# Optimization experiments

Measured on AMD Instinct MI355X. Metric: run time of the kernel, lower is better.

Reference implementation:

```python
import jax, jax.numpy as jnp
import numpy as np

D_MODEL = 768
N_HEADS = 12
D_HEAD = D_MODEL // N_HEADS


def setup_inputs() -> dict:
    key = jax.random.key(0)
    k_x, k_qw, k_qb, k_ow, k_ob = jax.random.split(key, 5)
    B, N = 2, 4096
    scale = 1.0 / np.sqrt(D_MODEL)
    return {
        "x": jax.random.normal(k_x, (B, N, D_MODEL), dtype=jnp.float32),
        # torch nn.Linear stores weight as [out_features, in_features]
        "qkv_w": jax.random.uniform(k_qw, (3 * D_MODEL, D_MODEL), jnp.float32, -scale, scale),
        "qkv_b": jax.random.uniform(k_qb, (3 * D_MODEL,), jnp.float32, -scale, scale),
        "out_w": jax.random.uniform(k_ow, (D_MODEL, D_MODEL), jnp.float32, -scale, scale),
        "out_b": jax.random.uniform(k_ob, (D_MODEL,), jnp.float32, -scale, scale),
    }


def reference(x, qkv_w, qkv_b, out_w, out_b):
    B, N, D = x.shape
    qkv = x @ qkv_w.T + qkv_b                                   # [B, N, 3D]
    qkv = qkv.reshape(B, N, 3, N_HEADS, D_HEAD)
    qkv = jnp.transpose(qkv, (2, 0, 3, 1, 4))                    # [3, B, H, N, d]
    q, k, v = qkv[0], qkv[1], qkv[2]
    scores = jnp.einsum("bhqd,bhkd->bhqk", q, k) / np.sqrt(D_HEAD)
    attn = jax.nn.softmax(scores, axis=-1)
    out = jnp.einsum("bhqk,bhkd->bhqd", attn, v)                 # [B, H, N, d]
    out = jnp.transpose(out, (0, 2, 1, 3)).reshape(B, N, D)
    return out @ out_w.T + out_b
```

## Files before the change

### kernel.cpp

```cpp
#include <hip/hip_runtime.h>
#include <cstdint>

#define SEQ 4096
#define NH 12
#define DH 64
#define DM 768
#define MT 8192
#define QKVN 2304

typedef __bf16 bf16;
typedef __attribute__((ext_vector_type(8))) __bf16 bf16x8;
typedef __attribute__((ext_vector_type(4))) __bf16 bf16x4;
typedef __attribute__((ext_vector_type(2))) __bf16 bf16x2;
typedef __attribute__((ext_vector_type(4))) float f32x4;
typedef __attribute__((ext_vector_type(16))) float f32x16;
typedef __attribute__((ext_vector_type(2))) int int2v;

__device__ __forceinline__ void async_ld16(const void* g, void* lds) {
  __builtin_amdgcn_global_load_lds(
      (__attribute__((address_space(1))) void*)(void*)g,
      (__attribute__((address_space(3))) void*)lds, 16, 0, 0);
}

__device__ __forceinline__ int pexp2_pair(float s0, float s1) {
  int j0 = (int)__builtin_fmaf(s0, 128.0f, 16251.5f);
  int j1 = (int)__builtin_fmaf(s1, 128.0f, 16251.5f);
  return j0 | (j1 << 16);
}

__device__ __forceinline__ void lane32_swap(int& a, int& b) {
#if __has_builtin(__builtin_amdgcn_permlane32_swap)
  int2v r = __builtin_amdgcn_permlane32_swap(a, b, false, false);
  a = r.x; b = r.y;
#else
  int hi = (threadIdx.x & 63) >> 5;
  int ra = __shfl_xor(a, 32, 64), rb = __shfl_xor(b, 32, 64);
  int na = hi ? rb : a;
  int nb = hi ? b : ra;
  a = na; b = nb;
#endif
}

#define NX4  (MT * DM / 4)
#define NW14 (QKVN * DM / 4)
#define NW24 (DM * DM / 4)
__global__ void cvt_all(const float* __restrict__ x, const float* __restrict__ w1,
                        const float* __restrict__ w2, bf16* __restrict__ xb,
                        bf16* __restrict__ wb1, bf16* __restrict__ wb2) {
  int i = blockIdx.x * blockDim.x + threadIdx.x;
  const float* src; bf16* dst; int j;
  if (i < NX4) { src = x; dst = xb; j = i; }
  else if (i < NX4 + NW14) { src = w1; dst = wb1; j = i - NX4; }
  else if (i < NX4 + NW14 + NW24) { src = w2; dst = wb2; j = i - NX4 - NW14; }
  else return;
  f32x4 v = ((const f32x4*)src)[j];
  bf16x4 o;
  o.x = (bf16)v.x; o.y = (bf16)v.y; o.z = (bf16)v.z; o.w = (bf16)v.w;
  ((bf16x4*)dst)[j] = o;
}

template<int MODE>
__global__ __launch_bounds__(256) void gemm_bt(
    const bf16* __restrict__ A, const bf16* __restrict__ Bw,
    const float* __restrict__ bias,
    bf16* __restrict__ outQ, bf16* __restrict__ outK, bf16* __restrict__ outVt,
    float* __restrict__ outF,
    int M, int N, int K)
{
  __shared__ bf16 smem[2 * 128 * 64];
  bf16* sA = smem;
  bf16* sB = smem + 128 * 64;
  bf16* sT = smem;

  const int tid  = threadIdx.x;
  const int wave = tid >> 6;
  const int lane = tid & 63;
  const int l15  = lane & 15;
  const int quad = lane >> 4;

  constexpr int NT = (MODE == 0) ? (QKVN / 128) : (DM / 128);
  const int lin = blockIdx.x;
  const int rem = lin % (NT * 8);
  const int m0 = ((lin / (NT * 8)) * 8 + (rem % 8)) * 128;
  const int n0 = (rem / 8) * 128;

  const int rowbase = (wave >> 1) * 64;
  const int colbase = (wave & 1) * 64;

  f32x4 acc[4][4] = {};

  const int srow = lane >> 3;
  const int spg  = (lane & 7) ^ srow;
  const int xk   = l15 & 7;

  for (int kt = 0; kt < K; kt += 64) {
#pragma unroll
    for (int p = 0; p < 8; ++p) {
      int chunk = p * 4 + wave;
      if (chunk < 16) {
        int row = chunk * 8 + srow;
        async_ld16(A + (size_t)(m0 + row) * K + kt + spg * 8, &sA[chunk * 512]);
      } else {
        int row = (chunk - 16) * 8 + srow;
        async_ld16(Bw + (size_t)(n0 + row) * K + kt + spg * 8, &sB[(chunk - 16) * 512]);
      }
    }
    __syncthreads();

#pragma unroll
    for (int ks = 0; ks < 2; ++ks) {
      bf16x8 af[4], bfr[4];
#pragma unroll
      for (int rt = 0; rt < 4; ++rt)
        af[rt] = *(const bf16x8*)&sA[(rowbase + rt * 16 + l15) * 64 +
                                     (((ks * 4 + quad) ^ xk) * 8)];
#pragma unroll
      for (int ct = 0; ct < 4; ++ct)
        bfr[ct] = *(const bf16x8*)&sB[(colbase + ct * 16 + l15) * 64 +
                                      (((ks * 4 + quad) ^ xk) * 8)];
#pragma unroll
      for (int rt = 0; rt < 4; ++rt)
#pragma unroll
        for (int ct = 0; ct < 4; ++ct)
          acc[rt][ct] = __builtin_amdgcn_mfma_f32_16x16x32_bf16(af[rt], bfr[ct], acc[rt][ct], 0, 0, 0);
    }
    __syncthreads();
  }

  if (MODE == 0) {
    const int g = n0 / DM;
    if (g < 2) {
      const float qscale = 0.125f * 1.4426950408889634f;
#pragma unroll
      for (int ct = 0; ct < 4; ++ct) {
        int j = n0 + colbase + ct * 16 + l15;
        float bj = bias[j];
        int f = j % DM;
        int h = f >> 6, d = f & 63;
#pragma unroll
        for (int rt = 0; rt < 4; ++rt) {
          int mrow = m0 + rowbase + rt * 16 + quad * 4;
#pragma unroll
          for (int r = 0; r < 4; ++r) {
            float v = acc[rt][ct][r] + bj;
            int m = mrow + r;
            int b = m >> 12, n = m & 4095;
            int bh = b * NH + h;
            if (g == 0) outQ[((size_t)bh * SEQ + n) * DH + d] = (bf16)(v * qscale);
            else        outK[((size_t)bh * SEQ + n) * DH + d] = (bf16)v;
          }
        }
      }
    } else {
      const int f0 = n0 - 2 * DM;
      const int b = m0 >> 12, n0m = m0 & 4095;
#pragma unroll
      for (int p = 0; p < 2; ++p) {
        __syncthreads();
        if (colbase == p * 64) {
#pragma unroll
          for (int ct = 0; ct < 4; ++ct) {
            int jl = ct * 16 + l15;
            float bj = bias[n0 + p * 64 + jl];
#pragma unroll
            for (int rt = 0; rt < 4; ++rt) {
              int ml = rowbase + rt * 16 + quad * 4;
#pragma unroll
              for (int r = 0; r < 4; ++r)
                sT[jl * 136 + ml + r] = (bf16)(acc[rt][ct][r] + bj);
            }
          }
        }
        __syncthreads();
#pragma unroll
        for (int p2 = 0; p2 < 4; ++p2) {
          int slot = p2 * 256 + tid;
          int jr = slot >> 4, mc = (slot & 15) * 8;
          int fj = f0 + p * 64 + jr;
          int h = fj >> 6, d = fj & 63;
          *(bf16x8*)&outVt[((size_t)(b * NH + h) * DH + d) * SEQ + n0m + mc] =
              *(const bf16x8*)&sT[jr * 136 + mc];
        }
      }
    }
  } else {
#pragma unroll
    for (int ct = 0; ct < 4; ++ct) {
      int j = n0 + colbase + ct * 16 + l15;
      float bj = bias[j];
#pragma unroll
      for (int rt = 0; rt < 4; ++rt) {
        int mrow = m0 + rowbase + rt * 16 + quad * 4;
#pragma unroll
        for (int r = 0; r < 4; ++r)
          outF[(size_t)(mrow + r) * N + j] = acc[rt][ct][r] + bj;
      }
    }
  }
}

__global__ __launch_bounds__(256) void flash_attn(
    const bf16* __restrict__ Q, const bf16* __restrict__ Kg,
    const bf16* __restrict__ Vt, bf16* __restrict__ Oout)
{
  __shared__ bf16 sK[2][64 * 64];
  __shared__ bf16 sV[2][64 * 64];

  {
    int ph = (blockIdx.x + blockIdx.y) & 3;
    if (ph == 1) __builtin_amdgcn_s_sleep(2);
    else if (ph == 2) __builtin_amdgcn_s_sleep(4);
    else if (ph == 3) __builtin_amdgcn_s_sleep(6);
  }

  const int tid  = threadIdx.x;
  const int wave = tid >> 6;
  const int lane = tid & 63;
  const int l31  = lane & 31;
  const int hi   = lane >> 5;
  const int bh = blockIdx.y;
  const int q0w = blockIdx.x * 128 + wave * 32;

  const bf16* Qb = Q  + (size_t)bh * SEQ * DH;
  const bf16* Kb = Kg + (size_t)bh * SEQ * DH;
  const bf16* Vb = Vt + (size_t)bh * DH * SEQ;

  const int srow = lane >> 3;
  const int spg  = lane & 7;

  bf16x8 qf[4];
#pragma unroll
  for (int dc = 0; dc < 4; ++dc)
    qf[dc] = *(const bf16x8*)&Qb[(size_t)(q0w + l31) * DH + dc * 16 + hi * 8];

  bf16x8 ones1;
#pragma unroll
  for (int j = 0; j < 8; ++j) ones1[j] = (bf16)1.0f;

  f32x16 o0 = {}, o1 = {}, o2 = {};
  f32x16 zc = {};

  const int keyk = (l31 & 7) ^ (((l31 >> 3) & 3) << 1);
  int kOff[4], vOff[4];
#pragma unroll
  for (int dc = 0; dc < 4; ++dc)
    kOff[dc] = l31 * 64 + (((dc * 2 + hi) ^ keyk) * 8);
#pragma unroll
  for (int k4 = 0; k4 < 4; ++k4)
    vOff[k4] = l31 * 64 + (((k4 * 2 + hi) ^ keyk) * 8);

  auto stage = [&](int kt, int buf) {
#pragma unroll
    for (int j = 0; j < 2; ++j) {
      int r0 = wave * 16 + j * 8;
      int row = r0 + srow;
      int lg = spg ^ (row & 7) ^ (((row >> 3) & 3) << 1);
      async_ld16(Kb + (size_t)(kt + row) * DH + lg * 8, &sK[buf][r0 * 64]);
      async_ld16(Vb + (size_t)row * SEQ + kt + lg * 8, &sV[buf][r0 * 64]);
    }
  };

  auto compute = [&](const bf16* sKp, const bf16* sVp) {
#pragma unroll
    for (int kb = 0; kb < 2; ++kb) {
      f32x16 s;
      {
        bf16x8 kf = *(const bf16x8*)&sKp[kOff[0] + kb * 2048];
        s = __builtin_amdgcn_mfma_f32_32x32x16_bf16(kf, qf[0], zc, 0, 0, 0);
      }
#pragma unroll
      for (int dc = 1; dc < 4; ++dc) {
        bf16x8 kf = *(const bf16x8*)&sKp[kOff[dc] + kb * 2048];
        s = __builtin_amdgcn_mfma_f32_32x32x16_bf16(kf, qf[dc], s, 0, 0, 0);
      }
#pragma unroll
      for (int kc = 0; kc < 2; ++kc) {
        int g0a = pexp2_pair(s[8 * kc + 0], s[8 * kc + 1]);
        int g0b = pexp2_pair(s[8 * kc + 2], s[8 * kc + 3]);
        int g1a = pexp2_pair(s[8 * kc + 4], s[8 * kc + 5]);
        int g1b = pexp2_pair(s[8 * kc + 6], s[8 * kc + 7]);
        lane32_swap(g0a, g1a);
        lane32_swap(g0b, g1b);
        union { int i[4]; bf16x8 v; } Af;
        Af.i[0] = g0a; Af.i[1] = g0b; Af.i[2] = g1a; Af.i[3] = g1b;
        bf16x8 vf0 = *(const bf16x8*)&sVp[vOff[kb * 2 + kc]];
        bf16x8 vf1 = *(const bf16x8*)&sVp[vOff[kb * 2 + kc] + 2048];
        o0 = __builtin_amdgcn_mfma_f32_32x32x16_bf16(Af.v, vf0, o0, 0, 0, 0);
        o1 = __builtin_amdgcn_mfma_f32_32x32x16_bf16(Af.v, vf1, o1, 0, 0, 0);
        o2 = __builtin_amdgcn_mfma_f32_32x32x16_bf16(Af.v, ones1, o2, 0, 0, 0);
      }
    }
  };

  stage(0, 0);
  __syncthreads();

  for (int kt = 0; kt < SEQ; kt += 128) {
    if (kt + 64 < SEQ) stage(kt + 64, 1);
    compute(sK[0], sV[0]);
    __syncthreads();
    if (kt + 128 < SEQ) stage(kt + 128, 0);
    compute(sK[1], sV[1]);
    __syncthreads();
  }

  const int bg = bh / NH, h = bh % NH;
#pragma unroll
  for (int i = 0; i < 16; ++i) {
    int ql = 8 * (i >> 2) + (i & 3) + 4 * hi;
    float inv = 1.0f / o2[i];
    size_t base = (size_t)(bg * SEQ + q0w + ql) * DM + h * DH;
    Oout[base + l31]      = (bf16)(o0[i] * inv);
    Oout[base + 32 + l31] = (bf16)(o1[i] * inv);
  }
}

extern "C" void kernel_launch(void* const* d_in, const int* in_sizes, int n_in,
                              void* d_out, int out_size, void* d_ws, size_t ws_size,
                              hipStream_t stream) {
  const float* x     = (const float*)d_in[0];
  const float* qkv_w = (const float*)d_in[1];
  const float* qkv_b = (const float*)d_in[2];
  const float* out_w = (const float*)d_in[3];
  const float* out_b = (const float*)d_in[4];
  float* out = (float*)d_out;

  char* w = (char*)d_ws;
  bf16* xb    = (bf16*)w; w += (size_t)MT * DM * 2;
  bf16* wqkv  = (bf16*)w; w += (size_t)QKVN * DM * 2;
  bf16* wout  = (bf16*)w; w += (size_t)DM * DM * 2;
  bf16* Qw    = (bf16*)w; w += (size_t)MT * DM * 2;
  bf16* Kw    = (bf16*)w; w += (size_t)MT * DM * 2;
  bf16* Vtw   = (bf16*)w; w += (size_t)MT * DM * 2;
  bf16* attnV = (bf16*)w; w += (size_t)MT * DM * 2;

  const int tot4 = NX4 + NW14 + NW24;
  cvt_all<<<dim3((tot4 + 255) / 256), 256, 0, stream>>>(x, qkv_w, out_w, xb, wqkv, wout);

  gemm_bt<0><<<dim3((QKVN / 128) * (MT / 128)), 256, 0, stream>>>(
      xb, wqkv, qkv_b, Qw, Kw, Vtw, nullptr, MT, QKVN, DM);

  flash_attn<<<dim3(SEQ / 128, 2 * NH), 256, 0, stream>>>(Qw, Kw, Vtw, attnV);

  gemm_bt<1><<<dim3((DM / 128) * (MT / 128)), 256, 0, stream>>>(
      attnV, wout, out_b, nullptr, nullptr, nullptr, out, MT, DM, DM);
}
```

Measured before the change: 268.8 us.

## Replace ones-MFMA row-sum with VALU accumulation, remap blocks across XCDs

Removes the third MFMA per PV step, which multiplied P by a ones matrix to get row sums. Row sums are now accumulated in registers from fp32 exp2 bit patterns truncated to bf16, then combined across lane halves with a shuffle. Exp2 becomes a float-exponent bit trick with a perm-based pack into bf16 pairs. Also remaps the block index so each XCD handles contiguous heads for better L2 reuse of K/V, and adds an occupancy hint of 3 blocks per CU. The extra VALU adds and shuffles are traded against the saved matrix-core work.

```diff
diff --git a/kernel.cpp b/kernel.cpp
--- a/kernel.cpp
+++ b/kernel.cpp
@@ -22,10 +22,16 @@
       (__attribute__((address_space(3))) void*)lds, 16, 0, 0);
 }
 
-__device__ __forceinline__ int pexp2_pair(float s0, float s1) {
-  int j0 = (int)__builtin_fmaf(s0, 128.0f, 16251.5f);
-  int j1 = (int)__builtin_fmaf(s1, 128.0f, 16251.5f);
-  return j0 | (j1 << 16);
+__device__ __forceinline__ int sexp2_bits(float s) {
+  return (int)__builtin_fmaf(s, 8388608.0f, 1065091072.0f);
+}
+
+__device__ __forceinline__ int pack_hi16(int lo, int hi) {
+#if __has_builtin(__builtin_amdgcn_perm)
+  return (int)__builtin_amdgcn_perm((unsigned)hi, (unsigned)lo, 0x07060302u);
+#else
+  return (int)(((unsigned)lo >> 16) | ((unsigned)hi & 0xffff0000u));
+#endif
 }
 
 __device__ __forceinline__ void lane32_swap(int& a, int& b) {
@@ -199,15 +205,21 @@
   }
 }
 
-__global__ __launch_bounds__(256) void flash_attn(
+__global__ __launch_bounds__(256, 3) void flash_attn(
     const bf16* __restrict__ Q, const bf16* __restrict__ Kg,
     const bf16* __restrict__ Vt, bf16* __restrict__ Oout)
 {
   __shared__ bf16 sK[2][64 * 64];
   __shared__ bf16 sV[2][64 * 64];
 
+  const int L    = blockIdx.x + (SEQ / 128) * blockIdx.y;
+  const int xcd  = L & 7;
+  const int slot = L >> 3;
+  const int bh   = xcd + 8 * (slot >> 5);
+  const int qb   = slot & 31;
+
   {
-    int ph = (blockIdx.x + blockIdx.y) & 3;
+    int ph = (qb + bh) & 3;
     if (ph == 1) __builtin_amdgcn_s_sleep(2);
     else if (ph == 2) __builtin_amdgcn_s_sleep(4);
     else if (ph == 3) __builtin_amdgcn_s_sleep(6);
@@ -218,8 +230,7 @@
   const int lane = tid & 63;
   const int l31  = lane & 31;
   const int hi   = lane >> 5;
-  const int bh = blockIdx.y;
-  const int q0w = blockIdx.x * 128 + wave * 32;
+  const int q0w = qb * 128 + wave * 32;
 
   const bf16* Qb = Q  + (size_t)bh * SEQ * DH;
   const bf16* Kb = Kg + (size_t)bh * SEQ * DH;
@@ -233,21 +244,14 @@
   for (int dc = 0; dc < 4; ++dc)
     qf[dc] = *(const bf16x8*)&Qb[(size_t)(q0w + l31) * DH + dc * 16 + hi * 8];
 
-  bf16x8 ones1;
-#pragma unroll
-  for (int j = 0; j < 8; ++j) ones1[j] = (bf16)1.0f;
-
-  f32x16 o0 = {}, o1 = {}, o2 = {};
-  f32x16 zc = {};
+  f32x16 o0 = {}, o1 = {};
+  float rs0 = 0.f, rs1 = 0.f, rs2 = 0.f, rs3 = 0.f;
 
   const int keyk = (l31 & 7) ^ (((l31 >> 3) & 3) << 1);
-  int kOff[4], vOff[4];
+  int off[4];
 #pragma unroll
   for (int dc = 0; dc < 4; ++dc)
-    kOff[dc] = l31 * 64 + (((dc * 2 + hi) ^ keyk) * 8);
-#pragma unroll
-  for (int k4 = 0; k4 < 4; ++k4)
-    vOff[k4] = l31 * 64 + (((k4 * 2 + hi) ^ keyk) * 8);
+    off[dc] = l31 * 64 + (((dc * 2 + hi) ^ keyk) * 8);
 
   auto stage = [&](int kt, int buf) {
 #pragma unroll
@@ -263,31 +267,38 @@
   auto compute = [&](const bf16* sKp, const bf16* sVp) {
 #pragma unroll
     for (int kb = 0; kb < 2; ++kb) {
-      f32x16 s;
-      {
-        bf16x8 kf = *(const bf16x8*)&sKp[kOff[0] + kb * 2048];
-        s = __builtin_amdgcn_mfma_f32_32x32x16_bf16(kf, qf[0], zc, 0, 0, 0);
-      }
-#pragma unroll
-      for (int dc = 1; dc < 4; ++dc) {
-        bf16x8 kf = *(const bf16x8*)&sKp[kOff[dc] + kb * 2048];
+      f32x16 s = {};
+#pragma unroll
+      for (int dc = 0; dc < 4; ++dc) {
+        bf16x8 kf = *(const bf16x8*)&sKp[off[dc] + kb * 2048];
         s = __builtin_amdgcn_mfma_f32_32x32x16_bf16(kf, qf[dc], s, 0, 0, 0);
       }
 #pragma unroll
       for (int kc = 0; kc < 2; ++kc) {
-        int g0a = pexp2_pair(s[8 * kc + 0], s[8 * kc + 1]);
-        int g0b = pexp2_pair(s[8 * kc + 2], s[8 * kc + 3]);
-        int g1a = pexp2_pair(s[8 * kc + 4], s[8 * kc + 5]);
-        int g1b = pexp2_pair(s[8 * kc + 6], s[8 * kc + 7]);
+        int b0 = sexp2_bits(s[8 * kc + 0]);
+        int b1 = sexp2_bits(s[8 * kc + 1]);
+        int b2 = sexp2_bits(s[8 * kc + 2]);
+        int b3 = sexp2_bits(s[8 * kc + 3]);
+        int b4 = sexp2_bits(s[8 * kc + 4]);
+        int b5 = sexp2_bits(s[8 * kc + 5]);
+        int b6 = sexp2_bits(s[8 * kc + 6]);
+        int b7 = sexp2_bits(s[8 * kc + 7]);
+        rs0 += __int_as_float(b0 & 0xffff0000) + __int_as_float(b4 & 0xffff0000);
+        rs1 += __int_as_float(b1 & 0xffff0000) + __int_as_float(b5 & 0xffff0000);
+        rs2 += __int_as_float(b2 & 0xffff0000) + __int_as_float(b6 & 0xffff0000);
+        rs3 += __int_as_float(b3 & 0xffff0000) + __int_as_float(b7 & 0xffff0000);
+        int g0a = pack_hi16(b0, b1);
+        int g0b = pack_hi16(b2, b3);
+        int g1a = pack_hi16(b4, b5);
+        int g1b = pack_hi16(b6, b7);
         lane32_swap(g0a, g1a);
         lane32_swap(g0b, g1b);
         union { int i[4]; bf16x8 v; } Af;
         Af.i[0] = g0a; Af.i[1] = g0b; Af.i[2] = g1a; Af.i[3] = g1b;
-        bf16x8 vf0 = *(const bf16x8*)&sVp[vOff[kb * 2 + kc]];
-        bf16x8 vf1 = *(const bf16x8*)&sVp[vOff[kb * 2 + kc] + 2048];
+        bf16x8 vf0 = *(const bf16x8*)&sVp[off[kb * 2 + kc]];
+        bf16x8 vf1 = *(const bf16x8*)&sVp[off[kb * 2 + kc] + 2048];
         o0 = __builtin_amdgcn_mfma_f32_32x32x16_bf16(Af.v, vf0, o0, 0, 0, 0);
         o1 = __builtin_amdgcn_mfma_f32_32x32x16_bf16(Af.v, vf1, o1, 0, 0, 0);
-        o2 = __builtin_amdgcn_mfma_f32_32x32x16_bf16(Af.v, ones1, o2, 0, 0, 0);
       }
     }
   };
@@ -304,11 +315,15 @@
     __syncthreads();
   }
 
+  float rsum = (rs0 + rs1) + (rs2 + rs3);
+  rsum += __shfl_xor(rsum, 32, 64);
+  float invq = 1.0f / rsum;
+
   const int bg = bh / NH, h = bh % NH;
 #pragma unroll
   for (int i = 0; i < 16; ++i) {
     int ql = 8 * (i >> 2) + (i & 3) + 4 * hi;
-    float inv = 1.0f / o2[i];
+    float inv = __shfl(invq, ql, 64);
     size_t base = (size_t)(bg * SEQ + q0w + ql) * DM + h * DH;
     Oout[base + l31]      = (bf16)(o0[i] * inv);
     Oout[base + 32 + l31] = (bf16)(o1[i] * inv);
```

Result: no change. 264.1 us (-1.7%).
